# Kernel tuning notes

Measured on AMD Instinct MI355X. Metric: run time of the kernel, lower is better.

Reference implementation:

```python
import jax, jax.numpy as jnp
import numpy as np

B, S, D = 2, 2048, 1024
H = 16
DK = D // H
FF = 4096
EPS = 1e-6


def setup_inputs() -> dict:
    key = jax.random.key(0)
    ks = jax.random.split(key, 16)
    sd = 0.02
    inp = {
        "x": jax.random.normal(ks[0], (B, S, D), dtype=jnp.float32),
        # attention projections (stored as [in, out]; y = x @ W + b)
        "Wq": jax.random.normal(ks[1], (D, D), dtype=jnp.float32) * sd,
        "bq": jnp.zeros((D,), jnp.float32),
        "Wk": jax.random.normal(ks[2], (D, D), dtype=jnp.float32) * sd,
        "bk": jnp.zeros((D,), jnp.float32),
        "Wv": jax.random.normal(ks[3], (D, D), dtype=jnp.float32) * sd,
        "bv": jnp.zeros((D,), jnp.float32),
        "Wo": jax.random.normal(ks[4], (D, D), dtype=jnp.float32) * sd,
        "bo": jnp.zeros((D,), jnp.float32),
        # FFN
        "W1": jax.random.normal(ks[5], (D, FF), dtype=jnp.float32) * sd,
        "b1": jnp.zeros((FF,), jnp.float32),
        "W2": jax.random.normal(ks[6], (FF, D), dtype=jnp.float32) * sd,
        "b2": jnp.zeros((D,), jnp.float32),
        # LayerNorms (pre-norm)
        "ln1_g": jnp.ones((D,), jnp.float32),
        "ln1_b": jnp.zeros((D,), jnp.float32),
        "ln2_g": jnp.ones((D,), jnp.float32),
        "ln2_b": jnp.zeros((D,), jnp.float32),
    }
    return inp


def _layer_norm(x, g, b):
    mu = jnp.mean(x, axis=-1, keepdims=True)
    var = jnp.mean(jnp.square(x - mu), axis=-1, keepdims=True)
    return (x - mu) * jax.lax.rsqrt(var + EPS) * g + b


def _attention(x, Wq, bq, Wk, bk, Wv, bv, Wo, bo):
    # project and split heads: [B,S,D] -> [B,H,S,DK]
    def split(t):
        return t.reshape(B, S, H, DK).transpose(0, 2, 1, 3)
    q = split(x @ Wq + bq)
    k = split(x @ Wk + bk)
    v = split(x @ Wv + bv)
    scores = jnp.einsum("bhqd,bhkd->bhqk", q, k) / jnp.sqrt(jnp.float32(DK))
    p = jax.nn.softmax(scores, axis=-1)  # no mask in forward path; dropout eval-mode
    o = jnp.einsum("bhqk,bhkd->bhqd", p, v)
    o = o.transpose(0, 2, 1, 3).reshape(B, S, D)
    return o @ Wo + bo


def reference(x, Wq, bq, Wk, bk, Wv, bv, Wo, bo, W1, b1, W2, b2,
              ln1_g, ln1_b, ln2_g, ln2_b):
    # sublayer 1: x + attn(LN(x))
    x = x + _attention(_layer_norm(x, ln1_g, ln1_b), Wq, bq, Wk, bk, Wv, bv, Wo, bo)
    # sublayer 2: x + FFN(LN(x))
    h = jax.nn.relu(_layer_norm(x, ln2_g, ln2_b) @ W1 + b1)
    x = x + (h @ W2 + b2)
    return x
```

## Files before the change

### kernel.cpp

```cpp
#include <hip/hip_runtime.h>


#define S_LEN 2048
#define DMODEL 1024
#define NHEADS 16
#define FFDIM 4096
#define MROWS 4096

typedef _Float16 f16;
typedef _Float16 f16x8 __attribute__((ext_vector_type(8)));
typedef __fp16 fp16x2 __attribute__((ext_vector_type(2)));
typedef float f32x4 __attribute__((ext_vector_type(4)));
typedef unsigned int u32;
typedef unsigned long long u64;
typedef unsigned long long u64x2 __attribute__((ext_vector_type(2)));

union Frag { f16x8 h; u64 q[2]; f16 e[8]; u32 w[4]; };

__device__ __forceinline__ f32x4 mfma16(f16x8 a, f16x8 b, f32x4 c) {
  return __builtin_amdgcn_mfma_f32_16x16x32_f16(a, b, c, 0, 0, 0);
}

__device__ __forceinline__ u32 pk16(float lo, float hi) {
  fp16x2 v = __builtin_amdgcn_cvt_pkrtz(lo, hi);
  return __builtin_bit_cast(u32, v);
}

typedef __attribute__((address_space(1))) const void gvoid;
typedef __attribute__((address_space(3))) void lvoid;

__device__ __forceinline__ void gload16(const f16* gp, f16* lp) {
  __builtin_amdgcn_global_load_lds((gvoid*)gp, (lvoid*)lp, 16, 0, 0);
}

__global__ __launch_bounds__(256) void wtrans4_kernel(const float* __restrict__ W0,
                                                      const float* __restrict__ W1,
                                                      const float* __restrict__ W2,
                                                      const float* __restrict__ W3,
                                                      f16* __restrict__ D0,
                                                      f16* __restrict__ D1,
                                                      f16* __restrict__ D2,
                                                      f16* __restrict__ D3) {
  const int z = blockIdx.z;
  const float* W = z == 0 ? W0 : z == 1 ? W1 : z == 2 ? W2 : W3;
  f16* Wt = z == 0 ? D0 : z == 1 ? D1 : z == 2 ? D2 : D3;
  __shared__ f16 tile[32][33];
  const int n0 = blockIdx.x * 32, k0 = blockIdx.y * 32;
  const int tx = threadIdx.x & 31, ty = threadIdx.x >> 5;
  for (int i = 0; i < 4; i++) {
    int k = ty + i * 8;
    tile[k][tx] = (f16)W[(size_t)(k0 + k) * 1024 + n0 + tx];
  }
  __syncthreads();
  for (int i = 0; i < 4; i++) {
    int n = ty + i * 8;
    Wt[(size_t)(n0 + n) * 1024 + k0 + tx] = tile[tx][n];
  }
}

__global__ __launch_bounds__(256) void wtrans2_kernel(const float* __restrict__ W1,
                                                      const float* __restrict__ W2,
                                                      f16* __restrict__ D1,
                                                      f16* __restrict__ D2) {
  const int z = blockIdx.z;
  const float* W = z ? W2 : W1;
  f16* Wt = z ? D2 : D1;
  const int K = z ? 4096 : 1024, N = z ? 1024 : 4096;
  const int n0 = (z ? blockIdx.y : blockIdx.x) * 32;
  const int k0 = (z ? blockIdx.x : blockIdx.y) * 32;
  __shared__ f16 tile[32][33];
  const int tx = threadIdx.x & 31, ty = threadIdx.x >> 5;
  for (int i = 0; i < 4; i++) {
    int k = ty + i * 8;
    tile[k][tx] = (f16)W[(size_t)(k0 + k) * N + n0 + tx];
  }
  __syncthreads();
  for (int i = 0; i < 4; i++) {
    int n = ty + i * 8;
    Wt[(size_t)(n0 + n) * K + k0 + tx] = tile[tx][n];
  }
}

__global__ void bias_concat_kernel(const float* __restrict__ bq,
                                   const float* __restrict__ bk,
                                   const float* __restrict__ bv,
                                   float* __restrict__ out) {
  int i = blockIdx.x * 256 + threadIdx.x;
  float v = (i < 1024) ? bq[i] : (i < 2048) ? bk[i - 1024] : bv[i - 2048];
  out[i] = v;
}

__global__ __launch_bounds__(256) void ln_kernel(const float* __restrict__ x,
                                                 const float* __restrict__ gw,
                                                 const float* __restrict__ bw,
                                                 f16* __restrict__ out) {
  const int row = blockIdx.x, t = threadIdx.x;
  const float* xr = x + (size_t)row * DMODEL;
  float4 v = *(const float4*)(xr + t * 4);
  float s = v.x + v.y + v.z + v.w;
  float s2 = v.x * v.x + v.y * v.y + v.z * v.z + v.w * v.w;
  for (int off = 1; off < 64; off <<= 1) {
    s += __shfl_xor(s, off);
    s2 += __shfl_xor(s2, off);
  }
  __shared__ float red[8];
  const int w = t >> 6, lane = t & 63;
  if (lane == 0) { red[w] = s; red[w + 4] = s2; }
  __syncthreads();
  s = red[0] + red[1] + red[2] + red[3];
  s2 = red[4] + red[5] + red[6] + red[7];
  float mu = s * (1.0f / DMODEL);
  float var = s2 * (1.0f / DMODEL) - mu * mu;
  float rstd = rsqrtf(var + 1e-6f);
  float4 g4 = *(const float4*)(gw + t * 4);
  float4 b4 = *(const float4*)(bw + t * 4);
  union { f16 h[4]; u64 q; } o;
  o.h[0] = (f16)((v.x - mu) * rstd * g4.x + b4.x);
  o.h[1] = (f16)((v.y - mu) * rstd * g4.y + b4.y);
  o.h[2] = (f16)((v.z - mu) * rstd * g4.z + b4.z);
  o.h[3] = (f16)((v.w - mu) * rstd * g4.w + b4.w);
  *(u64*)(out + (size_t)row * DMODEL + t * 4) = o.q;
}

template <int BM, int BN>
__global__ __launch_bounds__(256, 2) void gemm2(const f16* __restrict__ A, int lda,
                                                const f16* __restrict__ Bt, int ldb,
                                                const float* __restrict__ bias,
                                                const float* __restrict__ res,
                                                float* __restrict__ outf,
                                                f16* __restrict__ outh, int ldo,
                                                int N, int K, int relu) {
  constexpr int MT = BM / 32, NT = BN / 32;
  __shared__ f16 As[2][BM * 64];
  __shared__ f16 Bs[2][BN * 64];
  const int gx = gridDim.x;
  const int nwg = gx * gridDim.y;
  int id = blockIdx.y * gx + blockIdx.x;
  id = (id & 7) * (nwg >> 3) + (id >> 3);
  const int m0 = (id / gx) * BM, n0 = (id % gx) * BN;
  const int t = threadIdx.x;
  const int lane = t & 63, w = t >> 6;
  const int wr = w >> 1, wc = w & 1;
  const int rA = lane & 15, g = lane >> 4;

  f32x4 acc[MT][NT] = {};

  auto stageA = [&](int k0, int buf) {
#pragma unroll
    for (int p = 0; p < BM / 32; p++) {
      const int chunk = p * 256 + w * 64 + lane;
      const int row = chunk >> 3;
      const int cbg = ((chunk & 7) ^ (row & 7)) * 8;
      gload16(A + (size_t)(m0 + row) * lda + k0 + cbg,
              &As[buf][(p * 256 + w * 64) * 8]);
    }
  };
  auto stageB = [&](int k0, int buf) {
#pragma unroll
    for (int p = 0; p < BN / 32; p++) {
      const int chunk = p * 256 + w * 64 + lane;
      const int row = chunk >> 3;
      const int cbg = ((chunk & 7) ^ (row & 7)) * 8;
      gload16(Bt + (size_t)(n0 + row) * ldb + k0 + cbg,
              &Bs[buf][(p * 256 + w * 64) * 8]);
    }
  };

  auto compute = [&](int cur) {
#pragma unroll
    for (int ks = 0; ks < 2; ks++) {
      Frag a[MT], b[NT];
#pragma unroll
      for (int mt = 0; mt < MT; mt++) {
        const int row = wr * (BM / 2) + mt * 16 + rA;
        a[mt].h = *(const f16x8*)(&As[cur][row * 64 + ((ks * 4 + g) ^ (row & 7)) * 8]);
      }
#pragma unroll
      for (int nt = 0; nt < NT; nt++) {
        const int row = wc * (BN / 2) + nt * 16 + rA;
        b[nt].h = *(const f16x8*)(&Bs[cur][row * 64 + ((ks * 4 + g) ^ (row & 7)) * 8]);
      }
#pragma unroll
      for (int mt = 0; mt < MT; mt++)
#pragma unroll
        for (int nt = 0; nt < NT; nt++)
          acc[mt][nt] = mfma16(a[mt].h, b[nt].h, acc[mt][nt]);
    }
  };

  const int nsteps = K / 64;
  stageA(0, 0);
  stageB(0, 0);
  stageA(64, 1);

  for (int ts = 0; ts < nsteps - 1; ++ts) {
    const int cur = ts & 1;
    asm volatile("s_waitcnt vmcnt(4)" ::: "memory");
    __builtin_amdgcn_sched_barrier(0);
    __builtin_amdgcn_s_barrier();
    stageB(ts * 64 + 64, cur ^ 1);
    compute(cur);
    asm volatile("s_waitcnt lgkmcnt(0)" ::: "memory");
    __builtin_amdgcn_sched_barrier(0);
    __builtin_amdgcn_s_barrier();
    if (ts + 2 < nsteps) stageA(ts * 64 + 128, cur);
  }
  asm volatile("s_waitcnt vmcnt(0)" ::: "memory");
  __builtin_amdgcn_sched_barrier(0);
  __builtin_amdgcn_s_barrier();
  compute((nsteps - 1) & 1);

#pragma unroll
  for (int mt = 0; mt < MT; mt++) {
#pragma unroll
    for (int nt = 0; nt < NT; nt++) {
      const int col = n0 + wc * (BN / 2) + nt * 16 + rA;
      const int rowb = m0 + wr * (BM / 2) + mt * 16 + g * 4;
      const float bs = bias[col];
#pragma unroll
      for (int r = 0; r < 4; r++) {
        float v = acc[mt][nt][r] + bs;
        if (relu) v = fmaxf(v, 0.0f);
        if (res) v += res[(size_t)(rowb + r) * N + col];
        if (outf) outf[(size_t)(rowb + r) * N + col] = v;
        if (outh) outh[(size_t)(rowb + r) * ldo + col] = (f16)v;
      }
    }
  }
}

__global__ __launch_bounds__(256) void vtrans_kernel(const f16* __restrict__ qkv,
                                                     f16* __restrict__ vt) {
  const int bh = blockIdx.y;
  const int s0 = blockIdx.x * 64;
  const int b = bh >> 4, h = bh & 15;
  __shared__ f16 tile[64][72];
  const int t = threadIdx.x;
  for (int pass = 0; pass < 2; pass++) {
    int sl = (t >> 3) + pass * 32;
    int dk0 = (t & 7) * 8;
    u64x2 v = *(const u64x2*)(qkv + (size_t)(b * S_LEN + s0 + sl) * 3072 + 2048 + h * 64 + dk0);
    *(u64x2*)(&tile[sl][dk0]) = v;
  }
  __syncthreads();
  for (int pass = 0; pass < 2; pass++) {
    int dk = (t >> 3) + pass * 32;
    int sc = (t & 7) * 8;
    union { u64x2 q; f16 u[8]; } o;
    for (int j = 0; j < 8; j++) {
      int pos = sc + j;
      int kv = (pos & 32) | ((pos & 4) << 2) | ((pos & 0x18) >> 1) | (pos & 3);
      o.u[j] = tile[kv][dk];
    }
    *(u64x2*)(vt + (size_t)(bh * 64 + dk) * S_LEN + s0 + sc) = o.q;
  }
}

__global__ __launch_bounds__(256, 2) void attn_kernel(const f16* __restrict__ qkv,
                                                      const f16* __restrict__ vt,
                                                      f16* __restrict__ attn_out) {
  const int qt0 = blockIdx.x * 128;
  const int bh = blockIdx.y;
  const int b = bh >> 4, h = bh & 15;
  const int t = threadIdx.x;
  const int lane = t & 63, w = t >> 6;
  const int rA = lane & 15, g = lane >> 4;

  __shared__ f16 Ks[2][64 * 64];
  __shared__ f16 Vs[2][64 * 64];

  Frag qf[2][2];
#pragma unroll
  for (int qg = 0; qg < 2; qg++)
#pragma unroll
    for (int kt = 0; kt < 2; kt++) {
      const f16* p = qkv + (size_t)(b * S_LEN + qt0 + w * 32 + qg * 16 + rA) * 3072 +
                     h * 64 + kt * 32 + 8 * g;
      f16x8 v = *(const f16x8*)p;
#pragma unroll
      for (int j = 0; j < 8; j++) v[j] = v[j] * (f16)0.18033688f;
      qf[qg][kt].h = v;
    }

  float lRp[2] = {0.0f, 0.0f};
  f32x4 o2[2][4] = {};

#define STAGE_KV(kv0_, buf_)                                                     \
  {                                                                              \
    _Pragma("unroll") for (int i = 0; i < 2; i++) {                              \
      int C = i * 256 + w * 64 + lane;                                           \
      int row = C >> 3;                                                          \
      int cbg = ((C & 7) ^ (row & 7)) * 8;                                       \
      gload16(qkv + (size_t)(b * S_LEN + (kv0_) + row) * 3072 + 1024 + h * 64 + cbg, \
              &Ks[buf_][(i * 256 + w * 64) * 8]);                                \
      gload16(vt + (size_t)(bh * 64 + row) * S_LEN + (kv0_) + cbg,               \
              &Vs[buf_][(i * 256 + w * 64) * 8]);                                \
    }                                                                            \
  }

  int cur = 0;
  STAGE_KV(0, 0);

  for (int kv0 = 0; kv0 < S_LEN; kv0 += 64) {
    __syncthreads();
    if (kv0 + 64 < S_LEN) STAGE_KV(kv0 + 64, cur ^ 1);

    Frag kf[4][2];
#pragma unroll
    for (int nt = 0; nt < 4; nt++)
#pragma unroll
      for (int kt = 0; kt < 2; kt++) {
        const int row = nt * 16 + rA;
        kf[nt][kt].h = *(const f16x8*)(&Ks[cur][row * 64 + ((kt * 4 + g) ^ (row & 7)) * 8]);
      }
    f32x4 s[2][4] = {};
#pragma unroll
    for (int qg = 0; qg < 2; qg++)
#pragma unroll
      for (int nt = 0; nt < 4; nt++)
#pragma unroll
        for (int kt = 0; kt < 2; kt++)
          s[qg][nt] = mfma16(kf[nt][kt].h, qf[qg][kt].h, s[qg][nt]);

    Frag ph[2][2];
#pragma unroll
    for (int qg = 0; qg < 2; qg++) {
      float rs = 0.0f;
#pragma unroll
      for (int nt = 0; nt < 4; nt++)
#pragma unroll
        for (int r = 0; r < 4; r++) {
          float e0 = exp2f(s[qg][nt][r]);
          s[qg][nt][r] = e0;
          rs += e0;
        }
      lRp[qg] += rs;
#pragma unroll
      for (int j = 0; j < 2; j++) {
        ph[qg][j].w[0] = pk16(s[qg][2 * j][0], s[qg][2 * j][1]);
        ph[qg][j].w[1] = pk16(s[qg][2 * j][2], s[qg][2 * j][3]);
        ph[qg][j].w[2] = pk16(s[qg][2 * j + 1][0], s[qg][2 * j + 1][1]);
        ph[qg][j].w[3] = pk16(s[qg][2 * j + 1][2], s[qg][2 * j + 1][3]);
      }
    }

#pragma unroll
    for (int ntd = 0; ntd < 4; ntd++) {
      const int row = ntd * 16 + rA;
#pragma unroll
      for (int j = 0; j < 2; j++) {
        Frag vf;
        vf.h = *(const f16x8*)(&Vs[cur][row * 64 + ((j * 4 + g) ^ (row & 7)) * 8]);
#pragma unroll
        for (int qg = 0; qg < 2; qg++)
          o2[qg][ntd] = mfma16(vf.h, ph[qg][j].h, o2[qg][ntd]);
      }
    }

    cur ^= 1;
  }

#pragma unroll
  for (int qg = 0; qg < 2; qg++) {
    float l = lRp[qg];
    l += __shfl_xor(l, 16);
    l += __shfl_xor(l, 32);
    const float inv = 1.0f / l;
    const int qrow = qt0 + w * 32 + qg * 16 + rA;
#pragma unroll
    for (int ntd = 0; ntd < 4; ntd++) {
      union { f16 h[4]; u64 q; } pk;
#pragma unroll
      for (int r = 0; r < 4; r++) pk.h[r] = (f16)(o2[qg][ntd][r] * inv);
      *(u64*)(attn_out + (size_t)(b * S_LEN + qrow) * DMODEL + h * 64 + ntd * 16 + g * 4) = pk.q;
    }
  }
#undef STAGE_KV
}

extern "C" void kernel_launch(void* const* d_in, const int* in_sizes, int n_in,
                              void* d_out, int out_size, void* d_ws, size_t ws_size,
                              hipStream_t stream) {
  const float* x     = (const float*)d_in[0];
  const float* Wq    = (const float*)d_in[1];
  const float* bq    = (const float*)d_in[2];
  const float* Wk    = (const float*)d_in[3];
  const float* bk    = (const float*)d_in[4];
  const float* Wv    = (const float*)d_in[5];
  const float* bv    = (const float*)d_in[6];
  const float* Wo    = (const float*)d_in[7];
  const float* bo    = (const float*)d_in[8];
  const float* W1    = (const float*)d_in[9];
  const float* b1    = (const float*)d_in[10];
  const float* W2    = (const float*)d_in[11];
  const float* b2    = (const float*)d_in[12];
  const float* ln1g  = (const float*)d_in[13];
  const float* ln1b  = (const float*)d_in[14];
  const float* ln2g  = (const float*)d_in[15];
  const float* ln2b  = (const float*)d_in[16];
  float* out = (float*)d_out;
  char* ws = (char*)d_ws;

  size_t off = 0;
  f16* wqkv_t = (f16*)(ws + off); off += (size_t)3072 * 1024 * 2;
  f16* wo_t   = (f16*)(ws + off); off += (size_t)1024 * 1024 * 2;
  f16* w1_t   = (f16*)(ws + off); off += (size_t)4096 * 1024 * 2;
  f16* w2_t   = (f16*)(ws + off); off += (size_t)1024 * 4096 * 2;
  float* bqkv = (float*)(ws + off); off += 3072 * 4;
  f16* regB   = (f16*)(ws + off); off += (size_t)MROWS * 1024 * 2;
  f16* qkv    = (f16*)(ws + off); off += (size_t)MROWS * 3072 * 2;
  f16* vt     = (f16*)(ws + off); off += (size_t)MROWS * 1024 * 2;
  f16* hbuf   = qkv;

  wtrans4_kernel<<<dim3(32, 32, 4), 256, 0, stream>>>(
      Wq, Wk, Wv, Wo,
      wqkv_t, wqkv_t + (size_t)1024 * 1024, wqkv_t + (size_t)2048 * 1024, wo_t);
  wtrans2_kernel<<<dim3(128, 32, 2), 256, 0, stream>>>(W1, W2, w1_t, w2_t);
  bias_concat_kernel<<<12, 256, 0, stream>>>(bq, bk, bv, bqkv);

  ln_kernel<<<MROWS, 256, 0, stream>>>(x, ln1g, ln1b, regB);

  gemm2<128, 192><<<dim3(16, 32), 256, 0, stream>>>(regB, 1024, wqkv_t, 1024, bqkv,
                                                    nullptr, nullptr, qkv, 3072,
                                                    3072, 1024, 0);
  vtrans_kernel<<<dim3(32, 32), 256, 0, stream>>>(qkv, vt);

  attn_kernel<<<dim3(16, 32), 256, 0, stream>>>(qkv, vt, regB);

  gemm2<128, 64><<<dim3(16, 32), 256, 0, stream>>>(regB, 1024, wo_t, 1024, bo,
                                                   x, out, nullptr, 0,
                                                   1024, 1024, 0);
  ln_kernel<<<MROWS, 256, 0, stream>>>(out, ln2g, ln2b, regB);

  gemm2<128, 128><<<dim3(32, 32), 256, 0, stream>>>(regB, 1024, w1_t, 1024, b1,
                                                    nullptr, nullptr, hbuf, 4096,
                                                    4096, 1024, 1);
  gemm2<128, 64><<<dim3(16, 32), 256, 0, stream>>>(hbuf, 4096, w2_t, 4096, b2,
                                                   out, out, nullptr, 0,
                                                   1024, 4096, 0);
}
```

Measured before the change: 270.3 us.

## Add 256x256-tile 8-wave GEMM kernel for QKV and FFN1 projections

Introduces a new GEMM kernel with 512 threads and 256x256 output tiles, double-buffered LDS staging with XOR swizzle, and uses it for the QKV projection and the first FFN matmul. The larger tile raises arithmetic intensity and reduces redundant global loads of A and B per output element. In exchange it uses 128KB of LDS per block and a large accumulator array, which limits occupancy. The grid shrinks to 192 and 256 workgroups, risking underutilization of the 256 CUs on MI355X.

New measurement: 261.1 us. 3.4% less time.

```diff
diff --git a/kernel.cpp b/kernel.cpp
--- a/kernel.cpp
+++ b/kernel.cpp
@@ -120,6 +120,105 @@
   o.h[2] = (f16)((v.z - mu) * rstd * g4.z + b4.z);
   o.h[3] = (f16)((v.w - mu) * rstd * g4.w + b4.w);
   *(u64*)(out + (size_t)row * DMODEL + t * 4) = o.q;
+}
+
+__global__ __launch_bounds__(512, 2) void gemm8(const f16* __restrict__ A, int lda,
+                                                const f16* __restrict__ Bt, int ldb,
+                                                const float* __restrict__ bias,
+                                                f16* __restrict__ outh, int ldo,
+                                                int K, int relu) {
+  __shared__ f16 As[2][256 * 64];
+  __shared__ f16 Bs[2][256 * 64];
+  const int gx = gridDim.x;
+  const int nwg = gx * gridDim.y;
+  int id = blockIdx.y * gx + blockIdx.x;
+  id = (id & 7) * (nwg >> 3) + (id >> 3);
+  const int m0 = (id / gx) * 256, n0 = (id % gx) * 256;
+  const int t = threadIdx.x;
+  const int lane = t & 63, w = t >> 6;
+  const int wr = w >> 2, wc = w & 3;
+  const int rA = lane & 15, g = lane >> 4;
+
+  f32x4 acc[8][4] = {};
+
+  auto stageA = [&](int ts, int buf) {
+    const int k0 = ts * 64;
+#pragma unroll
+    for (int p = 0; p < 4; p++) {
+      const int chunk = p * 512 + t;
+      const int row = chunk >> 3;
+      const int cbg = ((chunk & 7) ^ (row & 7)) * 8;
+      gload16(A + (size_t)(m0 + row) * lda + k0 + cbg,
+              &As[buf][(p * 512 + w * 64) * 8]);
+    }
+  };
+  auto stageB = [&](int ts, int buf) {
+    const int k0 = ts * 64;
+#pragma unroll
+    for (int p = 0; p < 4; p++) {
+      const int chunk = p * 512 + t;
+      const int row = chunk >> 3;
+      const int cbg = ((chunk & 7) ^ (row & 7)) * 8;
+      gload16(Bt + (size_t)(n0 + row) * ldb + k0 + cbg,
+              &Bs[buf][(p * 512 + w * 64) * 8]);
+    }
+  };
+
+  auto compute = [&](int cur) {
+#pragma unroll
+    for (int ks = 0; ks < 2; ks++) {
+      Frag b[4];
+#pragma unroll
+      for (int nt = 0; nt < 4; nt++) {
+        const int row = wc * 64 + nt * 16 + rA;
+        b[nt].h = *(const f16x8*)(&Bs[cur][row * 64 + ((ks * 4 + g) ^ (row & 7)) * 8]);
+      }
+#pragma unroll
+      for (int mt = 0; mt < 8; mt++) {
+        const int row = wr * 128 + mt * 16 + rA;
+        Frag a;
+        a.h = *(const f16x8*)(&As[cur][row * 64 + ((ks * 4 + g) ^ (row & 7)) * 8]);
+#pragma unroll
+        for (int nt = 0; nt < 4; nt++)
+          acc[mt][nt] = mfma16(a.h, b[nt].h, acc[mt][nt]);
+      }
+    }
+  };
+
+  const int nt_steps = K / 64;
+  stageA(0, 0); stageB(0, 0);
+  stageA(1, 1); stageB(1, 1);
+
+  for (int ts = 0; ts < nt_steps; ++ts) {
+    const int cur = ts & 1;
+    if (ts + 1 < nt_steps)
+      asm volatile("s_waitcnt vmcnt(8)" ::: "memory");
+    else
+      asm volatile("s_waitcnt vmcnt(0)" ::: "memory");
+    __builtin_amdgcn_sched_barrier(0);
+    __builtin_amdgcn_s_barrier();
+    compute(cur);
+    asm volatile("s_waitcnt lgkmcnt(0)" ::: "memory");
+    __builtin_amdgcn_sched_barrier(0);
+    __builtin_amdgcn_s_barrier();
+    if (ts + 2 < nt_steps) { stageA(ts + 2, cur); stageB(ts + 2, cur); }
+  }
+
+#pragma unroll
+  for (int mt = 0; mt < 8; mt++) {
+#pragma unroll
+    for (int nt = 0; nt < 4; nt++) {
+      const int col = n0 + wc * 64 + nt * 16 + rA;
+      const int rowb = m0 + wr * 128 + mt * 16 + g * 4;
+      const float bs = bias[col];
+#pragma unroll
+      for (int r = 0; r < 4; r++) {
+        float v = acc[mt][nt][r] + bs;
+        if (relu) v = fmaxf(v, 0.0f);
+        outh[(size_t)(rowb + r) * ldo + col] = (f16)v;
+      }
+    }
+  }
 }
 
 template <int BM, int BN>
@@ -420,9 +519,8 @@
 
   ln_kernel<<<MROWS, 256, 0, stream>>>(x, ln1g, ln1b, regB);
 
-  gemm2<128, 192><<<dim3(16, 32), 256, 0, stream>>>(regB, 1024, wqkv_t, 1024, bqkv,
-                                                    nullptr, nullptr, qkv, 3072,
-                                                    3072, 1024, 0);
+  gemm8<<<dim3(12, 16), 512, 0, stream>>>(regB, 1024, wqkv_t, 1024, bqkv,
+                                          qkv, 3072, 1024, 0);
   vtrans_kernel<<<dim3(32, 32), 256, 0, stream>>>(qkv, vt);
 
   attn_kernel<<<dim3(16, 32), 256, 0, stream>>>(qkv, vt, regB);
@@ -432,9 +530,8 @@
                                                    1024, 1024, 0);
   ln_kernel<<<MROWS, 256, 0, stream>>>(out, ln2g, ln2b, regB);
 
-  gemm2<128, 128><<<dim3(32, 32), 256, 0, stream>>>(regB, 1024, w1_t, 1024, b1,
-                                                    nullptr, nullptr, hbuf, 4096,
-                                                    4096, 1024, 1);
+  gemm8<<<dim3(16, 16), 512, 0, stream>>>(regB, 1024, w1_t, 1024, b1,
+                                          hbuf, 4096, 1024, 1);
   gemm2<128, 64><<<dim3(16, 32), 256, 0, stream>>>(hbuf, 4096, w2_t, 4096, b2,
                                                    out, out, nullptr, 0,
                                                    1024, 4096, 0);
```
